# Kernel optimization log

Measured on AMD Instinct MI355X. Metric: run time of the kernel, lower is better.

The kernel has to match this reference:

```python
import jax, jax.numpy as jnp
import numpy as np

BOUNDS = 1.6
FEAT = 32
BASE = 128
MULTS = [1, 2, 4]
N = 300000


def setup_inputs() -> dict:
    key = jax.random.key(0)
    ks = jax.random.split(key, 10)
    inp = {"pts": jax.random.normal(ks[0], (N, 3), dtype=jnp.float32)}
    i = 1
    for l, m in enumerate(MULTS):
        R = BASE * m
        for p in range(3):
            inp[f"g{l}{p}"] = jax.random.uniform(ks[i], (FEAT, R, R), minval=0.1, maxval=0.5, dtype=jnp.float32)
            i += 1
    return inp


def bilinear_sample(grid, coords):
    # grid: [C,H,W]; coords: [N,2] in [-1,1], coords[:,0] -> x (W axis), coords[:,1] -> y (H axis)
    # matches F.grid_sample(mode='bilinear', padding_mode='border', align_corners=True)
    C, H, W = grid.shape
    x = jnp.clip((coords[:, 0] + 1.0) * 0.5 * (W - 1), 0.0, W - 1)
    y = jnp.clip((coords[:, 1] + 1.0) * 0.5 * (H - 1), 0.0, H - 1)
    x0 = jnp.floor(x)
    y0 = jnp.floor(y)
    wx = x - x0
    wy = y - y0
    x0i = x0.astype(jnp.int32)
    y0i = y0.astype(jnp.int32)
    x1i = jnp.minimum(x0i + 1, W - 1)
    y1i = jnp.minimum(y0i + 1, H - 1)
    v00 = grid[:, y0i, x0i]  # [C,N]
    v01 = grid[:, y0i, x1i]
    v10 = grid[:, y1i, x0i]
    v11 = grid[:, y1i, x1i]
    out = (v00 * (1.0 - wx) + v01 * wx) * (1.0 - wy) + (v10 * (1.0 - wx) + v11 * wx) * wy
    return out.T  # [N,C]


def reference(pts, g00, g01, g02, g10, g11, g12, g20, g21, g22):
    # normalize_aabb with aabb = [[b,b,b],[-b,-b,-b]] -> (pts-b)*(2/(-2b)) - 1
    p = (pts - BOUNDS) * (2.0 / (-2.0 * BOUNDS)) - 1.0
    # coordinate planes per matMode rows [0,1,1],[1,0,1],[1,1,0]
    planes = [p[:, (1, 2)], p[:, (0, 2)], p[:, (0, 1)]]
    grids = [[g00, g01, g02], [g10, g11, g12], [g20, g21, g22]]
    feats = []
    for level in grids:
        for idx in range(3):
            feats.append(bilinear_sample(level[idx], planes[idx]))
    return jnp.concatenate(feats, axis=-1)  # [N, 3*levels*FEAT]
```

## Files before the change

kernel.cpp:

```cpp
#include <hip/hip_runtime.h>
#include <hip/hip_fp16.h>


struct GridPtrs { const float* g[9]; };
struct GridOffs { size_t off[9]; };

__global__ __launch_bounds__(256) void transpose_grids_h_kernel(
    GridPtrs gp, GridOffs go, __half* __restrict__ t)
{
    const int b = blockIdx.y;
    const int l = b / 3;
    const int R = 128 << l;
    const int T = R * R;

    const int tid  = blockIdx.x * 256 + threadIdx.x;
    const int ch   = tid & 31;
    const int t0   = (tid >> 5) * 16;
    if (t0 >= T) return;

    const float* __restrict__ src = gp.g[b] + (size_t)ch * (size_t)T + t0;
    __half* __restrict__ dst = t + go.off[b];

#pragma unroll
    for (int i = 0; i < 16; ++i) {
        dst[(size_t)(t0 + i) * 32 + ch] = __float2half_rn(src[i]);
    }
}

__device__ __forceinline__ void h8_to_f(const uint4 u, float f[8])
{
    const __half2* h = (const __half2*)&u;
#pragma unroll
    for (int i = 0; i < 4; ++i) {
        const float2 t = __half22float2(h[i]);
        f[2 * i + 0] = t.x;
        f[2 * i + 1] = t.y;
    }
}

__global__ __launch_bounds__(256) void triplane_sample_h_kernel(
    const float* __restrict__ pts,
    const __half* __restrict__ tg,
    GridOffs go,
    float* __restrict__ out,
    int n_pts)
{
    const int tid = blockIdx.x * 256 + threadIdx.x;
    const int total = n_pts * 36;
    if (tid >= total) return;

    const int n  = tid / 36;
    const int r  = tid - n * 36;
    const int b  = r >> 2;
    const int ch = (r & 3) << 3;
    const int l  = (b >= 6) ? 2 : (b >= 3 ? 1 : 0);
    const int p  = b - l * 3;

    const float vx = pts[n * 3 + 0];
    const float vy = pts[n * 3 + 1];
    const float vz = pts[n * 3 + 2];

    const float scale = 2.0f / (-2.0f * 1.6f);
    const float px = (vx - 1.6f) * scale - 1.0f;
    const float py = (vy - 1.6f) * scale - 1.0f;
    const float pz = (vz - 1.6f) * scale - 1.0f;

    const float cx = (p == 0) ? py : px;
    const float cy = (p == 2) ? py : pz;

    const int   R   = 128 << l;
    const float Rm1 = (float)(R - 1);

    float x = (cx + 1.0f) * 0.5f * Rm1;
    float y = (cy + 1.0f) * 0.5f * Rm1;
    x = fminf(fmaxf(x, 0.0f), Rm1);
    y = fminf(fmaxf(y, 0.0f), Rm1);

    const float x0f = floorf(x);
    const float y0f = floorf(y);
    const float wx  = x - x0f;
    const float wy  = y - y0f;
    const int x0 = (int)x0f;
    const int y0 = (int)y0f;
    const int x1 = min(x0 + 1, R - 1);
    const int y1 = min(y0 + 1, R - 1);

    const __half* base = tg + go.off[b] + ch;
    const size_t s00 = ((size_t)(y0 * R + x0)) * 32;
    const size_t s01 = ((size_t)(y0 * R + x1)) * 32;
    const size_t s10 = ((size_t)(y1 * R + x0)) * 32;
    const size_t s11 = ((size_t)(y1 * R + x1)) * 32;

    const uint4 u00 = *(const uint4*)(base + s00);
    const uint4 u01 = *(const uint4*)(base + s01);
    const uint4 u10 = *(const uint4*)(base + s10);
    const uint4 u11 = *(const uint4*)(base + s11);

    float f00[8], f01[8], f10[8], f11[8];
    h8_to_f(u00, f00);
    h8_to_f(u01, f01);
    h8_to_f(u10, f10);
    h8_to_f(u11, f11);

    const float omwx = 1.0f - wx;
    const float omwy = 1.0f - wy;

    float res[8];
#pragma unroll
    for (int k = 0; k < 8; ++k) {
        res[k] = (f00[k] * omwx + f01[k] * wx) * omwy
               + (f10[k] * omwx + f11[k] * wx) * wy;
    }

    float* op = out + (size_t)n * 288 + b * 32 + ch;
    *(float4*)(op + 0) = make_float4(res[0], res[1], res[2], res[3]);
    *(float4*)(op + 4) = make_float4(res[4], res[5], res[6], res[7]);
}

__global__ __launch_bounds__(256) void triplane_sample_kernel(
    const float* __restrict__ pts,
    GridPtrs gp,
    float* __restrict__ out,
    int n_pts)
{
    const int tid = blockIdx.x * 256 + threadIdx.x;
    const int total = n_pts * 72;
    if (tid >= total) return;

    const int n  = tid / 72;
    const int c4 = tid - n * 72;
    const int b  = c4 >> 3;
    const int ch = (c4 & 7) << 2;
    const int l  = (b >= 6) ? 2 : (b >= 3 ? 1 : 0);
    const int p  = b - l * 3;

    const float vx = pts[n * 3 + 0];
    const float vy = pts[n * 3 + 1];
    const float vz = pts[n * 3 + 2];

    const float scale = 2.0f / (-2.0f * 1.6f);
    const float px = (vx - 1.6f) * scale - 1.0f;
    const float py = (vy - 1.6f) * scale - 1.0f;
    const float pz = (vz - 1.6f) * scale - 1.0f;

    const float cx = (p == 0) ? py : px;
    const float cy = (p == 2) ? py : pz;

    const int   R   = 128 << l;
    const float Rm1 = (float)(R - 1);

    float x = (cx + 1.0f) * 0.5f * Rm1;
    float y = (cy + 1.0f) * 0.5f * Rm1;
    x = fminf(fmaxf(x, 0.0f), Rm1);
    y = fminf(fmaxf(y, 0.0f), Rm1);

    const float x0f = floorf(x);
    const float y0f = floorf(y);
    const float wx  = x - x0f;
    const float wy  = y - y0f;
    const int x0 = (int)x0f;
    const int y0 = (int)y0f;
    const int x1 = min(x0 + 1, R - 1);
    const int y1 = min(y0 + 1, R - 1);

    const size_t RR   = (size_t)R * (size_t)R;
    const float* base = gp.g[b] + (size_t)ch * RR;

    const int i00 = y0 * R + x0;
    const int i01 = y0 * R + x1;
    const int i10 = y1 * R + x0;
    const int i11 = y1 * R + x1;

    const float omwx = 1.0f - wx;
    const float omwy = 1.0f - wy;

    float rr[4];
#pragma unroll
    for (int k = 0; k < 4; ++k) {
        const float* gk = base + (size_t)k * RR;
        rr[k] = (gk[i00] * omwx + gk[i01] * wx) * omwy
              + (gk[i10] * omwx + gk[i11] * wx) * wy;
    }
    ((float4*)out)[tid] = make_float4(rr[0], rr[1], rr[2], rr[3]);
}

extern "C" void kernel_launch(void* const* d_in, const int* in_sizes, int n_in,
                              void* d_out, int out_size, void* d_ws, size_t ws_size,
                              hipStream_t stream)
{
    const float* pts = (const float*)d_in[0];
    GridPtrs gp;
    for (int i = 0; i < 9; ++i) gp.g[i] = (const float*)d_in[1 + i];
    float* out = (float*)d_out;

    const int n_pts = in_sizes[0] / 3;
    const int block = 256;

    GridOffs go;
    size_t off = 0;
    for (int b = 0; b < 9; ++b) {
        go.off[b] = off;
        const int R = 128 << (b / 3);
        off += (size_t)32 * R * R;
    }
    const size_t needed_bytes = off * sizeof(__half);

    if (ws_size >= needed_bytes) {
        __half* tg = (__half*)d_ws;
        dim3 tgrid(2048, 9, 1);
        transpose_grids_h_kernel<<<tgrid, block, 0, stream>>>(gp, go, tg);
        const int total = n_pts * 36;
        const int grid  = (total + block - 1) / block;
        triplane_sample_h_kernel<<<grid, block, 0, stream>>>(pts, tg, go, out, n_pts);
    } else {
        const int total = n_pts * 72;
        const int grid  = (total + block - 1) / block;
        triplane_sample_kernel<<<grid, block, 0, stream>>>(pts, gp, out, n_pts);
    }
}
```

Baseline: 565.2 us.

## Sort points by Morton key before sampling to improve grid locality

Adds a counting-sort pipeline (zero, histogram with atomics, single-block scan, scatter) that buckets points into a 32^3 Morton order. The sampling kernel then walks points in sorted order through a permutation, so neighbouring threads read nearby grid texels and cache hit rates should rise. The cost is four extra launches, atomic contention on dense buckets, a serial 1024-thread scan, and output writes scattered by point index instead of contiguous. Workspace needs grow by the count, cursor and permutation buffers, so the fallback path may trigger if the workspace is small.

```diff
diff --git a/kernel.cpp b/kernel.cpp
--- a/kernel.cpp
+++ b/kernel.cpp
@@ -4,6 +4,80 @@
 
 struct GridPtrs { const float* g[9]; };
 struct GridOffs { size_t off[9]; };
+
+#define NBUCKETS 32768
+
+__global__ __launch_bounds__(256) void zero_counts_kernel(int* __restrict__ counts)
+{
+    const int i = blockIdx.x * 256 + threadIdx.x;
+    if (i < NBUCKETS) counts[i] = 0;
+}
+
+__device__ __forceinline__ unsigned expand3(unsigned v)
+{
+    return (v & 1u) | ((v & 2u) << 2) | ((v & 4u) << 4) |
+           ((v & 8u) << 6) | ((v & 16u) << 8);
+}
+
+__device__ __forceinline__ unsigned morton_key(float vx, float vy, float vz)
+{
+    const float s = 32.0f / 3.2f;
+    int cx = (int)((vx + 1.6f) * s);
+    int cy = (int)((vy + 1.6f) * s);
+    int cz = (int)((vz + 1.6f) * s);
+    cx = min(max(cx, 0), 31);
+    cy = min(max(cy, 0), 31);
+    cz = min(max(cz, 0), 31);
+    return expand3((unsigned)cx) | (expand3((unsigned)cy) << 1) | (expand3((unsigned)cz) << 2);
+}
+
+__global__ __launch_bounds__(256) void histogram_kernel(
+    const float* __restrict__ pts, int* __restrict__ counts, int n_pts)
+{
+    const int n = blockIdx.x * 256 + threadIdx.x;
+    if (n >= n_pts) return;
+    const unsigned k = morton_key(pts[n * 3 + 0], pts[n * 3 + 1], pts[n * 3 + 2]);
+    atomicAdd(&counts[k], 1);
+}
+
+__global__ __launch_bounds__(1024) void scan_kernel(
+    const int* __restrict__ counts, int* __restrict__ cursor)
+{
+    __shared__ int part[1024];
+    const int t = threadIdx.x;
+    int local[32];
+    int s = 0;
+#pragma unroll
+    for (int i = 0; i < 32; ++i) {
+        local[i] = s;
+        s += counts[t * 32 + i];
+    }
+    part[t] = s;
+    __syncthreads();
+    for (int d = 1; d < 1024; d <<= 1) {
+        const int v   = part[t];
+        const int add = (t >= d) ? part[t - d] : 0;
+        __syncthreads();
+        part[t] = v + add;
+        __syncthreads();
+    }
+    const int base = (t == 0) ? 0 : part[t - 1];
+#pragma unroll
+    for (int i = 0; i < 32; ++i) {
+        cursor[t * 32 + i] = base + local[i];
+    }
+}
+
+__global__ __launch_bounds__(256) void scatter_kernel(
+    const float* __restrict__ pts, int* __restrict__ cursor,
+    int* __restrict__ perm, int n_pts)
+{
+    const int n = blockIdx.x * 256 + threadIdx.x;
+    if (n >= n_pts) return;
+    const unsigned k = morton_key(pts[n * 3 + 0], pts[n * 3 + 1], pts[n * 3 + 2]);
+    const int pos = atomicAdd(&cursor[k], 1);
+    perm[pos] = n;
+}
 
 __global__ __launch_bounds__(256) void transpose_grids_h_kernel(
     GridPtrs gp, GridOffs go, __half* __restrict__ t)
@@ -42,6 +116,7 @@
     const float* __restrict__ pts,
     const __half* __restrict__ tg,
     GridOffs go,
+    const int* __restrict__ perm,
     float* __restrict__ out,
     int n_pts)
 {
@@ -49,8 +124,9 @@
     const int total = n_pts * 36;
     if (tid >= total) return;
 
-    const int n  = tid / 36;
-    const int r  = tid - n * 36;
+    const int s  = tid / 36;
+    const int r  = tid - s * 36;
+    const int n  = perm[s];
     const int b  = r >> 2;
     const int ch = (r & 3) << 3;
     const int l  = (b >= 6) ? 2 : (b >= 3 ? 1 : 0);
@@ -203,15 +279,29 @@
         const int R = 128 << (b / 3);
         off += (size_t)32 * R * R;
     }
-    const size_t needed_bytes = off * sizeof(__half);
+
+    const size_t tg_bytes     = ((off * sizeof(__half)) + 255) & ~(size_t)255;
+    const size_t counts_bytes = (size_t)NBUCKETS * 4;
+    const size_t needed_bytes = tg_bytes + 2 * counts_bytes + (size_t)n_pts * 4;
 
     if (ws_size >= needed_bytes) {
-        __half* tg = (__half*)d_ws;
+        char* wsb   = (char*)d_ws;
+        __half* tg  = (__half*)wsb;
+        int* counts = (int*)(wsb + tg_bytes);
+        int* cursor = (int*)(wsb + tg_bytes + counts_bytes);
+        int* perm   = (int*)(wsb + tg_bytes + 2 * counts_bytes);
+
+        zero_counts_kernel<<<(NBUCKETS + 255) / 256, block, 0, stream>>>(counts);
+        histogram_kernel<<<(n_pts + 255) / 256, block, 0, stream>>>(pts, counts, n_pts);
+        scan_kernel<<<1, 1024, 0, stream>>>(counts, cursor);
+        scatter_kernel<<<(n_pts + 255) / 256, block, 0, stream>>>(pts, cursor, perm, n_pts);
+
         dim3 tgrid(2048, 9, 1);
         transpose_grids_h_kernel<<<tgrid, block, 0, stream>>>(gp, go, tg);
+
         const int total = n_pts * 36;
         const int grid  = (total + block - 1) / block;
-        triplane_sample_h_kernel<<<grid, block, 0, stream>>>(pts, tg, go, out, n_pts);
+        triplane_sample_h_kernel<<<grid, block, 0, stream>>>(pts, tg, go, perm, out, n_pts);
     } else {
         const int total = n_pts * 72;
         const int grid  = (total + block - 1) / block;
```

After: 598.5 us. +5.9%, slower.

## Use LDS-tiled transpose for fp16 grid conversion and nontemporal output stores

Applied to the files above, without the earlier changes.

Rewrites the grid transpose kernel to stage a 64-texel by 32-channel tile in shared memory. Reads from the source become vectorized nontemporal loads and writes become 16-byte stores, replacing the strided 2-byte scattered writes. The sampling kernel's output writes become nontemporal stores so they do not pollute the cache. The transpose grid is doubled so it covers the 64-texel tiles.

```diff
diff --git a/kernel.cpp b/kernel.cpp
--- a/kernel.cpp
+++ b/kernel.cpp
@@ -2,8 +2,13 @@
 #include <hip/hip_fp16.h>
 
 
+typedef float        f32x4 __attribute__((ext_vector_type(4)));
+typedef unsigned int u32x4 __attribute__((ext_vector_type(4)));
+
 struct GridPtrs { const float* g[9]; };
 struct GridOffs { size_t off[9]; };
+
+#define TP_TEX 64
 
 __global__ __launch_bounds__(256) void transpose_grids_h_kernel(
     GridPtrs gp, GridOffs go, __half* __restrict__ t)
@@ -13,17 +18,41 @@
     const int R = 128 << l;
     const int T = R * R;
 
-    const int tid  = blockIdx.x * 256 + threadIdx.x;
-    const int ch   = tid & 31;
-    const int t0   = (tid >> 5) * 16;
-    if (t0 >= T) return;
-
-    const float* __restrict__ src = gp.g[b] + (size_t)ch * (size_t)T + t0;
-    __half* __restrict__ dst = t + go.off[b];
-
-#pragma unroll
-    for (int i = 0; i < 16; ++i) {
-        dst[(size_t)(t0 + i) * 32 + ch] = __float2half_rn(src[i]);
+    const int tile0 = blockIdx.x * TP_TEX;
+    if (tile0 >= T) return;
+
+    __shared__ unsigned short lds[TP_TEX * 33];
+
+    const int tid = threadIdx.x;
+
+    {
+        const int ch   = tid >> 3;
+        const int part = (tid & 7) << 3;
+        const float* __restrict__ src = gp.g[b] + (size_t)ch * (size_t)T + tile0 + part;
+        const f32x4 a0 = __builtin_nontemporal_load((const f32x4*)src);
+        const f32x4 a1 = __builtin_nontemporal_load((const f32x4*)(src + 4));
+#pragma unroll
+        for (int k = 0; k < 4; ++k)
+            lds[(part + k) * 33 + ch] = __half_as_ushort(__float2half_rn(a0[k]));
+#pragma unroll
+        for (int k = 0; k < 4; ++k)
+            lds[(part + 4 + k) * 33 + ch] = __half_as_ushort(__float2half_rn(a1[k]));
+    }
+    __syncthreads();
+
+    {
+        const int tex = tid >> 2;
+        const int q   = (tid & 3) << 3;
+        const unsigned short* row = &lds[tex * 33 + q];
+        u32x4 v;
+#pragma unroll
+        for (int k = 0; k < 4; ++k) {
+            const unsigned lo = row[2 * k];
+            const unsigned hi = row[2 * k + 1];
+            v[k] = lo | (hi << 16);
+        }
+        __half* dst = t + go.off[b] + (size_t)(tile0 + tex) * 32 + q;
+        *(u32x4*)dst = v;
     }
 }
 
@@ -113,8 +142,10 @@
     }
 
     float* op = out + (size_t)n * 288 + b * 32 + ch;
-    *(float4*)(op + 0) = make_float4(res[0], res[1], res[2], res[3]);
-    *(float4*)(op + 4) = make_float4(res[4], res[5], res[6], res[7]);
+    const f32x4 r0 = {res[0], res[1], res[2], res[3]};
+    const f32x4 r1 = {res[4], res[5], res[6], res[7]};
+    __builtin_nontemporal_store(r0, (f32x4*)op);
+    __builtin_nontemporal_store(r1, (f32x4*)(op + 4));
 }
 
 __global__ __launch_bounds__(256) void triplane_sample_kernel(
@@ -207,7 +238,7 @@
 
     if (ws_size >= needed_bytes) {
         __half* tg = (__half*)d_ws;
-        dim3 tgrid(2048, 9, 1);
+        dim3 tgrid(4096, 9, 1);
         transpose_grids_h_kernel<<<tgrid, block, 0, stream>>>(gp, go, tg);
         const int total = n_pts * 36;
         const int grid  = (total + block - 1) / block;
```

Measured after the change: 551.4 us. 1.03x faster.
